# Kernel optimization log

Measured on AMD Instinct MI355X. Metric: run time of the kernel, lower is better.

## Reference

```python
import jax, jax.numpy as jnp
import numpy as np

NUM_GROUPS = 17
NUM_OCCLUDED = 10
TEMP = 0.1


def setup_inputs() -> dict:
    key = jax.random.key(0)
    k1, k2 = jax.random.split(key)
    B, N, D = 128, 577, 768
    x = jax.random.normal(k1, (B, N, D), dtype=jnp.float32)
    # xavier_uniform-like scale for (D, G) weight
    bound = float(np.sqrt(6.0 / (D + NUM_GROUPS)))
    group_weights = jax.random.uniform(k2, (D, NUM_GROUPS), dtype=jnp.float32, minval=-bound, maxval=bound)
    return {"x": x, "group_weights": group_weights}


def _l2_normalize(v):
    # matches F.normalize(dim=-1, eps=1e-12)
    return v / jnp.maximum(jnp.linalg.norm(v, axis=-1, keepdims=True), 1e-12)


def reference(x, group_weights):
    B, N, D = x.shape
    cls_token = x[:, 0, :]            # (B, D)
    patch_tokens = x[:, 1:, :]        # (B, P, D), P = N-1

    # cosine similarity of each patch with cls token
    sim = jnp.einsum('bpd,bd->bp', _l2_normalize(patch_tokens), _l2_normalize(cls_token))  # (B, P)

    # k least-similar patches are "occluded" -> zero them out
    _, occ_idx = jax.lax.top_k(-sim, NUM_OCCLUDED)  # (B, K)
    mask = jnp.ones_like(sim).at[jnp.arange(B)[:, None], occ_idx].set(0.0)  # (B, P)
    non_occ = patch_tokens * mask[..., None]  # (B, P, D)

    # attention-style group pooling; softmax over groups (dim=1)
    scores = jnp.einsum('dg,bpd->bgp', group_weights, non_occ) / TEMP  # (B, G, P)
    attn = jax.nn.softmax(scores, axis=1)
    group_features = jnp.einsum('bgp,bpd->bgd', attn, non_occ)  # (B, G, D)

    # pack [global_feat, group_feat_1..G] as (B, 1+G, D)
    feats = jnp.concatenate([cls_token[:, None, :], group_features], axis=1)
    return feats, attn
```

## Files before the change

### kernel.cpp

```cpp
#include <hip/hip_runtime.h>
#include <math.h>

#define B_ 128
#define NTOK 577
#define P_ 576
#define D_ 768
#define G_ 17
#define KOCC 10
#define INV_TEMP 10.0f
#define U17 (1.0f / 17.0f)
#define NCHUNK 9

#define OFF_WT 0
#define OFF_SIM (G_ * D_)
#define OFF_CLSINV (OFF_SIM + B_ * P_)
#define OFF_GFP (OFF_CLSINV + B_)
#define GFP_PART ((size_t)B_ * G_ * D_)

__global__ __launch_bounds__(256) void k0_cls(const float* __restrict__ x,
                                              const float* __restrict__ gw,
                                              float* __restrict__ feats,
                                              float* __restrict__ clsinv,
                                              float* __restrict__ wt,
                                              int zero_groups) {
    if (blockIdx.x >= B_) {
        int g = blockIdx.x - B_;
        for (int d = threadIdx.x; d < D_; d += 256)
            wt[g * D_ + d] = gw[d * G_ + g];
        return;
    }
    int b = blockIdx.x;
    const float* cls = x + (size_t)b * NTOK * D_;
    float* fb = feats + (size_t)b * 18 * D_;
    float ss = 0.f;
    for (int i = threadIdx.x; i < D_ / 4; i += 256) {
        float4 v = ((const float4*)cls)[i];
        ((float4*)fb)[i] = v;
        ss = fmaf(v.x, v.x, fmaf(v.y, v.y, fmaf(v.z, v.z, fmaf(v.w, v.w, ss))));
    }
    if (zero_groups) {
        float4 z = {0.f, 0.f, 0.f, 0.f};
        for (int i = threadIdx.x; i < G_ * D_ / 4; i += 256)
            ((float4*)(fb + D_))[i] = z;
    }
    #pragma unroll
    for (int off = 32; off; off >>= 1) ss += __shfl_xor(ss, off, 64);
    __shared__ float red[4];
    int wave = threadIdx.x >> 6, lane = threadIdx.x & 63;
    if (lane == 0) red[wave] = ss;
    __syncthreads();
    if (threadIdx.x == 0) {
        float t = red[0] + red[1] + red[2] + red[3];
        clsinv[b] = 1.0f / fmaxf(sqrtf(t), 1e-12f);
    }
}

__global__ __launch_bounds__(512) void k1_score(const float* __restrict__ x,
                                                const float* __restrict__ wt,
                                                const float* __restrict__ clsinv,
                                                float* __restrict__ sim,
                                                float* __restrict__ attn) {
    __shared__ __align__(16) float atile[19 * 68];
    int tid = threadIdx.x;
    int b = blockIdx.y, chunk = blockIdx.x;
    const float* clsrow = x + (size_t)b * NTOK * D_;

    int lane = tid & 63, wave = tid >> 6;
    int lr = lane & 15, rh = lane >> 4;
    int lr4 = lr * 4;
    int pbase = wave * 8 + rh * 2;
    const float* xp0 = x + ((size_t)(b * NTOK + 1 + chunk * 64 + pbase)) * D_ + lr4;
    const float* cp  = clsrow + lr4;

    float4 xv[2], xn[2], cv, cn;
    xv[0] = *(const float4*)(xp0);
    xv[1] = *(const float4*)(xp0 + D_);
    cv = *(const float4*)(cp);
    xn[0] = xv[0]; xn[1] = xv[1]; cn = cv;

    float s[19][2];
    #pragma unroll
    for (int i = 0; i < 19; ++i) { s[i][0] = 0.f; s[i][1] = 0.f; }

    for (int kc = 0; kc < 12; ++kc) {
        if (kc < 11) {
            xn[0] = *(const float4*)(xp0 + (kc + 1) * 64);
            xn[1] = *(const float4*)(xp0 + (kc + 1) * 64 + D_);
            cn = *(const float4*)(cp + (kc + 1) * 64);
        }
        const float* wk = wt + kc * 64 + lr4;
        #pragma unroll
        for (int g = 0; g < 17; ++g) {
            float4 w4 = *(const float4*)(wk + (size_t)g * D_);
            #pragma unroll
            for (int m = 0; m < 2; ++m)
                s[g][m] = fmaf(xv[m].x, w4.x, fmaf(xv[m].y, w4.y,
                          fmaf(xv[m].z, w4.z, fmaf(xv[m].w, w4.w, s[g][m]))));
        }
        #pragma unroll
        for (int m = 0; m < 2; ++m)
            s[17][m] = fmaf(xv[m].x, cv.x, fmaf(xv[m].y, cv.y,
                       fmaf(xv[m].z, cv.z, fmaf(xv[m].w, cv.w, s[17][m]))));
        #pragma unroll
        for (int m = 0; m < 2; ++m)
            s[18][m] = fmaf(xv[m].x, xv[m].x, fmaf(xv[m].y, xv[m].y,
                       fmaf(xv[m].z, xv[m].z, fmaf(xv[m].w, xv[m].w, s[18][m]))));
        xv[0] = xn[0]; xv[1] = xn[1]; cv = cn;
    }

    #pragma unroll
    for (int off = 8; off >= 1; off >>= 1)
        #pragma unroll
        for (int i = 0; i < 19; ++i)
            #pragma unroll
            for (int m = 0; m < 2; ++m)
                s[i][m] += __shfl_xor(s[i][m], off, 16);

    #pragma unroll
    for (int g = 0; g < 19; ++g) {
        if (lr == ((g < 16) ? g : 15)) {
            float2 v = {s[g][0], s[g][1]};
            *(float2*)&atile[g * 68 + pbase] = v;
        }
    }
    __syncthreads();

    if (tid < 64) {
        int p = chunk * 64 + tid;
        float v[17];
        float mx = -3.0e38f;
        #pragma unroll
        for (int g = 0; g < 17; ++g) {
            v[g] = atile[g * 68 + tid];
            mx = fmaxf(mx, v[g]);
        }
        float tot = 0.f;
        #pragma unroll
        for (int g = 0; g < 17; ++g) {
            v[g] = __expf((v[g] - mx) * INV_TEMP);
            tot += v[g];
        }
        float inv = 1.0f / tot;
        float* ap = attn + ((size_t)b * G_) * P_ + p;
        #pragma unroll
        for (int g = 0; g < 17; ++g) ap[(size_t)g * P_] = v[g] * inv;
        float cd = atile[17 * 68 + tid];
        float sq = atile[18 * 68 + tid];
        sim[(size_t)b * P_ + p] = cd * clsinv[b] / fmaxf(sqrtf(sq), 1e-12f);
    }
}

__global__ __launch_bounds__(192) void k3_pv(const float* __restrict__ x,
                                             const float* __restrict__ attn,
                                             float* __restrict__ gfp,
                                             float* __restrict__ feats,
                                             int use_part) {
    __shared__ __align__(16) float am[17 * 68];
    int tid = threadIdx.x;
    int chunk = blockIdx.x, b = blockIdx.y;

    for (int i = tid; i < 17 * 64; i += 192) {
        int g = i >> 6, p = i & 63;
        am[g * 68 + p] = attn[((size_t)b * G_ + g) * P_ + chunk * 64 + p];
    }
    __syncthreads();

    const float* xb = x + ((size_t)(b * NTOK) + 1 + chunk * 64) * D_ + tid * 4;
    float4 acc[G_];
    #pragma unroll
    for (int g = 0; g < G_; ++g) acc[g] = make_float4(0.f, 0.f, 0.f, 0.f);

    float4 c0 = *(const float4*)(xb + (size_t)0 * D_);
    float4 c1 = *(const float4*)(xb + (size_t)1 * D_);
    float4 c2 = *(const float4*)(xb + (size_t)2 * D_);
    float4 c3 = *(const float4*)(xb + (size_t)3 * D_);

    for (int pp = 0; pp < 64; pp += 4) {
        float4 n0 = c0, n1 = c1, n2 = c2, n3 = c3;
        if (pp + 4 < 64) {
            n0 = *(const float4*)(xb + (size_t)(pp + 4) * D_);
            n1 = *(const float4*)(xb + (size_t)(pp + 5) * D_);
            n2 = *(const float4*)(xb + (size_t)(pp + 6) * D_);
            n3 = *(const float4*)(xb + (size_t)(pp + 7) * D_);
        }
        #pragma unroll
        for (int g = 0; g < G_; ++g) {
            float4 a = *(const float4*)&am[g * 68 + pp];
            acc[g].x = fmaf(a.x, c0.x, fmaf(a.y, c1.x, fmaf(a.z, c2.x, fmaf(a.w, c3.x, acc[g].x))));
            acc[g].y = fmaf(a.x, c0.y, fmaf(a.y, c1.y, fmaf(a.z, c2.y, fmaf(a.w, c3.y, acc[g].y))));
            acc[g].z = fmaf(a.x, c0.z, fmaf(a.y, c1.z, fmaf(a.z, c2.z, fmaf(a.w, c3.z, acc[g].z))));
            acc[g].w = fmaf(a.x, c0.w, fmaf(a.y, c1.w, fmaf(a.z, c2.w, fmaf(a.w, c3.w, acc[g].w))));
        }
        c0 = n0; c1 = n1; c2 = n2; c3 = n3;
    }

    if (use_part) {
        float* gb = gfp + ((size_t)(chunk * B_ + b) * G_) * D_ + tid * 4;
        #pragma unroll
        for (int g = 0; g < G_; ++g) *(float4*)(gb + (size_t)g * D_) = acc[g];
    } else {
        float* fb = feats + ((size_t)(b * 18) + 1) * D_ + tid * 4;
        #pragma unroll
        for (int g = 0; g < G_; ++g) {
            atomicAdd(fb + (size_t)g * D_ + 0, acc[g].x);
            atomicAdd(fb + (size_t)g * D_ + 1, acc[g].y);
            atomicAdd(fb + (size_t)g * D_ + 2, acc[g].z);
            atomicAdd(fb + (size_t)g * D_ + 3, acc[g].w);
        }
    }
}

__global__ __launch_bounds__(192) void k24_fin(const float* __restrict__ x,
                                               const float* __restrict__ sim,
                                               const float* __restrict__ gfp,
                                               float* __restrict__ attn,
                                               float* __restrict__ feats,
                                               int use_part) {
    __shared__ int s_occ[KOCC];
    __shared__ float s_a0[KOCC][G_];
    int b = blockIdx.x, tid = threadIdx.x;

    if (tid < 64) {
        int lane = tid;
        int base = lane * 9;
        float v[9];
        #pragma unroll
        for (int j = 0; j < 9; ++j) v[j] = sim[(size_t)b * P_ + base + j];
        for (int t = 0; t < KOCC; ++t) {
            float mv = 3.0e38f;
            int mi = 1 << 30;
            #pragma unroll
            for (int j = 0; j < 9; ++j) {
                if (v[j] < mv) { mv = v[j]; mi = base + j; }
            }
            #pragma unroll
            for (int off = 1; off < 64; off <<= 1) {
                float ov = __shfl_xor(mv, off, 64);
                int oi = __shfl_xor(mi, off, 64);
                if (ov < mv || (ov == mv && oi < mi)) { mv = ov; mi = oi; }
            }
            if (lane == 0) s_occ[t] = mi;
            int loc = mi - base;
            if (loc >= 0 && loc < 9) v[loc] = 3.0e38f;
        }
    }

    float4 acc[G_];
    float* fb = feats + ((size_t)(b * 18) + 1) * D_ + tid * 4;
    if (use_part) {
        #pragma unroll
        for (int g = 0; g < G_; ++g) acc[g] = make_float4(0.f, 0.f, 0.f, 0.f);
        for (int pc = 0; pc < NCHUNK; ++pc) {
            const float* gb = gfp + ((size_t)(pc * B_ + b) * G_) * D_ + tid * 4;
            #pragma unroll
            for (int g = 0; g < G_; ++g) {
                float4 v = *(const float4*)(gb + (size_t)g * D_);
                acc[g].x += v.x; acc[g].y += v.y; acc[g].z += v.z; acc[g].w += v.w;
            }
        }
    } else {
        #pragma unroll
        for (int g = 0; g < G_; ++g) acc[g] = *(const float4*)(fb + (size_t)g * D_);
    }
    __syncthreads();

    for (int i = tid; i < KOCC * G_; i += 192) {
        int t = i / G_, g = i - t * G_;
        size_t idx = ((size_t)b * G_ + g) * P_ + s_occ[t];
        s_a0[t][g] = attn[idx];
        attn[idx] = U17;
    }
    __syncthreads();

    #pragma unroll
    for (int t = 0; t < KOCC; ++t) {
        float4 xo = *(const float4*)(x + ((size_t)(b * NTOK) + 1 + s_occ[t]) * D_ + tid * 4);
        #pragma unroll
        for (int g = 0; g < G_; ++g) {
            float a0 = s_a0[t][g];
            acc[g].x = fmaf(-a0, xo.x, acc[g].x);
            acc[g].y = fmaf(-a0, xo.y, acc[g].y);
            acc[g].z = fmaf(-a0, xo.z, acc[g].z);
            acc[g].w = fmaf(-a0, xo.w, acc[g].w);
        }
    }
    #pragma unroll
    for (int g = 0; g < G_; ++g) *(float4*)(fb + (size_t)g * D_) = acc[g];
}

extern "C" void kernel_launch(void* const* d_in, const int* in_sizes, int n_in,
                              void* d_out, int out_size, void* d_ws, size_t ws_size,
                              hipStream_t stream) {
    const float* x  = (const float*)d_in[0];
    const float* gw = (const float*)d_in[1];
    float* feats = (float*)d_out;
    float* attn  = (float*)d_out + (size_t)B_ * 18 * D_;
    float* wt      = (float*)d_ws + OFF_WT;
    float* sim     = (float*)d_ws + OFF_SIM;
    float* clsinv  = (float*)d_ws + OFF_CLSINV;
    float* gfp     = (float*)d_ws + OFF_GFP;

    int use_part = (((size_t)OFF_GFP + (size_t)NCHUNK * GFP_PART) * sizeof(float) <= ws_size);

    k0_cls<<<B_ + G_, 256, 0, stream>>>(x, gw, feats, clsinv, wt, !use_part);
    k1_score<<<dim3(NCHUNK, B_), 512, 0, stream>>>(x, wt, clsinv, sim, attn);
    k3_pv<<<dim3(NCHUNK, B_), 192, 0, stream>>>(x, attn, gfp, feats, use_part);
    k24_fin<<<B_, 192, 0, stream>>>(x, sim, gfp, attn, feats, use_part);
}
```

Measured before the change: 451.8 us.

## Fuse score and group-pooling kernels, staging weights and cls row in LDS

Merges the score/softmax kernel and the attention-weighted pooling kernel into one launch. The softmax weights stay in shared memory instead of going through global memory, and the chunk of x just read is read again right away, while it is likely still cached. The group weights and the cls row are also copied into LDS once per block rather than read from global memory inside the inner loop. In exchange the block uses about 60KB of LDS, which limits occupancy. Only 192 of the 512 threads do the pooling phase, so most of the block sits idle during that phase.

```diff
diff --git a/kernel.cpp b/kernel.cpp
--- a/kernel.cpp
+++ b/kernel.cpp
@@ -55,12 +55,18 @@
     }
 }
 
-__global__ __launch_bounds__(512) void k1_score(const float* __restrict__ x,
-                                                const float* __restrict__ wt,
-                                                const float* __restrict__ clsinv,
-                                                float* __restrict__ sim,
-                                                float* __restrict__ attn) {
+__global__ __launch_bounds__(512) void k13_score_pv(const float* __restrict__ x,
+                                                    const float* __restrict__ wt,
+                                                    const float* __restrict__ clsinv,
+                                                    float* __restrict__ sim,
+                                                    float* __restrict__ attn,
+                                                    float* __restrict__ gfp,
+                                                    float* __restrict__ feats,
+                                                    int use_part) {
+    __shared__ __align__(16) float wlds[G_ * D_];
+    __shared__ __align__(16) float clds[D_];
     __shared__ __align__(16) float atile[19 * 68];
+
     int tid = threadIdx.x;
     int b = blockIdx.y, chunk = blockIdx.x;
     const float* clsrow = x + (size_t)b * NTOK * D_;
@@ -70,25 +76,30 @@
     int lr4 = lr * 4;
     int pbase = wave * 8 + rh * 2;
     const float* xp0 = x + ((size_t)(b * NTOK + 1 + chunk * 64 + pbase)) * D_ + lr4;
-    const float* cp  = clsrow + lr4;
-
-    float4 xv[2], xn[2], cv, cn;
+
+    float4 xv[2], xn[2];
     xv[0] = *(const float4*)(xp0);
     xv[1] = *(const float4*)(xp0 + D_);
-    cv = *(const float4*)(cp);
-    xn[0] = xv[0]; xn[1] = xv[1]; cn = cv;
+
+    for (int i = tid; i < G_ * D_ / 4; i += 512)
+        ((float4*)wlds)[i] = ((const float4*)wt)[i];
+    for (int i = tid; i < D_ / 4; i += 512)
+        ((float4*)clds)[i] = ((const float4*)clsrow)[i];
 
     float s[19][2];
     #pragma unroll
     for (int i = 0; i < 19; ++i) { s[i][0] = 0.f; s[i][1] = 0.f; }
+
+    xn[0] = xv[0]; xn[1] = xv[1];
+    __syncthreads();
 
     for (int kc = 0; kc < 12; ++kc) {
         if (kc < 11) {
             xn[0] = *(const float4*)(xp0 + (kc + 1) * 64);
             xn[1] = *(const float4*)(xp0 + (kc + 1) * 64 + D_);
-            cn = *(const float4*)(cp + (kc + 1) * 64);
-        }
-        const float* wk = wt + kc * 64 + lr4;
+        }
+        float4 cls4 = *(const float4*)&clds[kc * 64 + lr4];
+        const float* wk = wlds + kc * 64 + lr4;
         #pragma unroll
         for (int g = 0; g < 17; ++g) {
             float4 w4 = *(const float4*)(wk + (size_t)g * D_);
@@ -99,13 +110,13 @@
         }
         #pragma unroll
         for (int m = 0; m < 2; ++m)
-            s[17][m] = fmaf(xv[m].x, cv.x, fmaf(xv[m].y, cv.y,
-                       fmaf(xv[m].z, cv.z, fmaf(xv[m].w, cv.w, s[17][m]))));
+            s[17][m] = fmaf(xv[m].x, cls4.x, fmaf(xv[m].y, cls4.y,
+                       fmaf(xv[m].z, cls4.z, fmaf(xv[m].w, cls4.w, s[17][m]))));
         #pragma unroll
         for (int m = 0; m < 2; ++m)
             s[18][m] = fmaf(xv[m].x, xv[m].x, fmaf(xv[m].y, xv[m].y,
                        fmaf(xv[m].z, xv[m].z, fmaf(xv[m].w, xv[m].w, s[18][m]))));
-        xv[0] = xn[0]; xv[1] = xn[1]; cv = cn;
+        xv[0] = xn[0]; xv[1] = xn[1];
     }
 
     #pragma unroll
@@ -143,28 +154,18 @@
         float inv = 1.0f / tot;
         float* ap = attn + ((size_t)b * G_) * P_ + p;
         #pragma unroll
-        for (int g = 0; g < 17; ++g) ap[(size_t)g * P_] = v[g] * inv;
+        for (int g = 0; g < 17; ++g) {
+            float av = v[g] * inv;
+            ap[(size_t)g * P_] = av;
+            atile[g * 68 + tid] = av;
+        }
         float cd = atile[17 * 68 + tid];
         float sq = atile[18 * 68 + tid];
         sim[(size_t)b * P_ + p] = cd * clsinv[b] / fmaxf(sqrtf(sq), 1e-12f);
     }
-}
-
-__global__ __launch_bounds__(192) void k3_pv(const float* __restrict__ x,
-                                             const float* __restrict__ attn,
-                                             float* __restrict__ gfp,
-                                             float* __restrict__ feats,
-                                             int use_part) {
-    __shared__ __align__(16) float am[17 * 68];
-    int tid = threadIdx.x;
-    int chunk = blockIdx.x, b = blockIdx.y;
-
-    for (int i = tid; i < 17 * 64; i += 192) {
-        int g = i >> 6, p = i & 63;
-        am[g * 68 + p] = attn[((size_t)b * G_ + g) * P_ + chunk * 64 + p];
-    }
-    __syncthreads();
-
+    __syncthreads();
+
+    if (tid >= 192) return;
     const float* xb = x + ((size_t)(b * NTOK) + 1 + chunk * 64) * D_ + tid * 4;
     float4 acc[G_];
     #pragma unroll
@@ -185,7 +186,7 @@
         }
         #pragma unroll
         for (int g = 0; g < G_; ++g) {
-            float4 a = *(const float4*)&am[g * 68 + pp];
+            float4 a = *(const float4*)&atile[g * 68 + pp];
             acc[g].x = fmaf(a.x, c0.x, fmaf(a.y, c1.x, fmaf(a.z, c2.x, fmaf(a.w, c3.x, acc[g].x))));
             acc[g].y = fmaf(a.x, c0.y, fmaf(a.y, c1.y, fmaf(a.z, c2.y, fmaf(a.w, c3.y, acc[g].y))));
             acc[g].z = fmaf(a.x, c0.z, fmaf(a.y, c1.z, fmaf(a.z, c2.z, fmaf(a.w, c3.z, acc[g].z))));
@@ -303,7 +304,6 @@
     int use_part = (((size_t)OFF_GFP + (size_t)NCHUNK * GFP_PART) * sizeof(float) <= ws_size);
 
     k0_cls<<<B_ + G_, 256, 0, stream>>>(x, gw, feats, clsinv, wt, !use_part);
-    k1_score<<<dim3(NCHUNK, B_), 512, 0, stream>>>(x, wt, clsinv, sim, attn);
-    k3_pv<<<dim3(NCHUNK, B_), 192, 0, stream>>>(x, attn, gfp, feats, use_part);
+    k13_score_pv<<<dim3(NCHUNK, B_), 512, 0, stream>>>(x, wt, clsinv, sim, attn, gfp, feats, use_part);
     k24_fin<<<B_, 192, 0, stream>>>(x, sim, gfp, attn, feats, use_part);
 }
```

Measured after the change: 381.4 us. -15.6%, faster.
